# Kernel optimization log

Measured on AMD Instinct MI355X. Metric: run time of the kernel, lower is better.

The kernel has to match this reference:

```python
import jax, jax.numpy as jnp
import numpy as np

N = 100000   # num nodes
E = 2000000  # num edges
D = 32       # feature dim (input_dim == hidden)
L = 6        # num layers
R = 50       # num relations
B = 64       # num query source nodes
EPS = 1e-6


def setup_inputs() -> dict:
    key = jax.random.key(0)
    ks = jax.random.split(key, 7)
    edge_index = jax.random.randint(ks[0], (E, 2), 0, N)
    edge_type = jax.random.randint(ks[1], (E,), 0, R)
    edge_weight = jnp.ones((E,), jnp.float32)
    h_index = jax.random.randint(ks[2], (B,), 0, N)
    rel_emb = jax.random.normal(ks[3], (L, R, D), jnp.float32) * 0.1
    W = jax.random.normal(ks[4], (L, 13 * D, D), jnp.float32) * (1.0 / np.sqrt(13 * D))
    b = jnp.zeros((L, D), jnp.float32)
    return dict(edge_index=edge_index, edge_type=edge_type, edge_weight=edge_weight,
                h_index=h_index, rel_emb=rel_emb, W=W, b=b)


def _layer(x, boundary, node_in, node_out, edge_type, edge_weight, rel, W, b, degree_out):
    # message: distmult  (E, D)
    msg = x[node_in] * rel[edge_type]
    # append boundary as self-loop messages -> (E+N, D)
    msg = jnp.concatenate([msg, boundary], axis=0)
    seg = jnp.concatenate([node_out, jnp.arange(N)], axis=0)
    w = jnp.concatenate([edge_weight, jnp.ones((N,), x.dtype)], axis=0)[:, None]
    mw = msg * w
    cnt = jax.ops.segment_sum(jnp.ones_like(w), seg, num_segments=N)  # (N,1), >=1
    mean = jax.ops.segment_sum(mw, seg, num_segments=N) / cnt
    sq_mean = jax.ops.segment_sum((msg * msg) * w, seg, num_segments=N) / cnt
    mx = jax.ops.segment_max(mw, seg, num_segments=N)
    mn = jax.ops.segment_min(mw, seg, num_segments=N)
    std = jnp.sqrt(jnp.clip(sq_mean - mean * mean, EPS, None))
    # interleave per-channel [mean, max, min, std] -> (N, 4D)
    feat = jnp.stack([mean, mx, mn, std], axis=-1).reshape(N, 4 * D)
    scale = jnp.log(degree_out)              # (N, 1)
    scale = scale / scale.mean()
    scales = jnp.concatenate([jnp.ones_like(scale), scale,
                              1.0 / jnp.clip(scale, 1e-2, None)], axis=-1)  # (N, 3)
    update = (feat[:, :, None] * scales[:, None, :]).reshape(N, 12 * D)
    out = jnp.concatenate([x, update], axis=-1) @ W + b  # (N, D)
    return jax.nn.relu(out)


def reference(edge_index, edge_type, edge_weight, h_index, rel_emb, W, b):
    node_in = edge_index[:, 0]
    node_out = edge_index[:, 1]
    boundary = jnp.zeros((N, D), jnp.float32).at[h_index].set(1.0)
    degree_out = (jax.ops.segment_sum(edge_weight, node_out, num_segments=N) + 1.0)[:, None]
    x = boundary
    for i in range(L):
        x = _layer(x, boundary, node_in, node_out, edge_type, edge_weight,
                   rel_emb[i], W[i], b[i], degree_out)
    return x  # node_feature (N, D)
```

## Files before the change

### kernel.cpp

```cpp
#include <hip/hip_runtime.h>
#include <math.h>

#define NN 100000
#define EE 2000000
#define DD 32
#define LL 6
#define RR 50
#define BB 64
#define SCAN_BLK 98


typedef __attribute__((ext_vector_type(8))) short bf16x8;
typedef __attribute__((ext_vector_type(4))) float f32x4;

__device__ __forceinline__ unsigned short f2bf(float f) {
    unsigned int u = __float_as_uint(f);
    u = (u + 0x7FFFu + ((u >> 16) & 1u)) >> 16;
    return (unsigned short)u;
}
__device__ __forceinline__ float bf2f(unsigned short h) {
    return __uint_as_float((unsigned int)h << 16);
}

__global__ void hist_kernel(const int* __restrict__ ei, int* __restrict__ cnt) {
    for (int e = blockIdx.x * blockDim.x + threadIdx.x; e < EE; e += gridDim.x * blockDim.x)
        atomicAdd(&cnt[ei[2 * e + 1]], 1);
}

__global__ void boundary_kernel(const int* __restrict__ h, float* __restrict__ bnd,
                                float* __restrict__ x0, unsigned short* __restrict__ xbf0) {
    int t = blockIdx.x * blockDim.x + threadIdx.x;
    if (t >= BB * DD) return;
    int bidx = t >> 5, d = t & 31;
    int node = h[bidx];
    x0[node * DD + d] = 1.0f;
    if (xbf0) xbf0[node * DD + d] = 0x3F80;
    if (d == 0) bnd[node] = 1.0f;
}

__global__ void scanA_kernel(const int* __restrict__ cnt, int* __restrict__ rowptr,
                             int* __restrict__ bsum) {
    __shared__ int sh[1024];
    const int idx = blockIdx.x * 1024 + threadIdx.x;
    const int v = (idx < NN) ? cnt[idx] : 0;
    sh[threadIdx.x] = v;
    __syncthreads();
    for (int off = 1; off < 1024; off <<= 1) {
        int t = (threadIdx.x >= (unsigned)off) ? sh[threadIdx.x - off] : 0;
        __syncthreads();
        sh[threadIdx.x] += t;
        __syncthreads();
    }
    if (idx < NN) rowptr[idx] = sh[threadIdx.x] - v;
    if (threadIdx.x == 1023) bsum[blockIdx.x] = sh[1023];
}

__global__ void scanB_kernel(const int* __restrict__ bsum, int* __restrict__ boff,
                             int* __restrict__ rowptr) {
    __shared__ int sh[128];
    const int t = threadIdx.x;
    const int v = (t < SCAN_BLK) ? bsum[t] : 0;
    sh[t] = v;
    __syncthreads();
    for (int off = 1; off < 128; off <<= 1) {
        int u = (t >= off) ? sh[t - off] : 0;
        __syncthreads();
        sh[t] += u;
        __syncthreads();
    }
    if (t < SCAN_BLK) boff[t] = sh[t] - v;
    if (t == SCAN_BLK - 1) rowptr[NN] = sh[t];
}

__global__ void scanC_kernel(int* __restrict__ rowptr, int* __restrict__ cursor,
                             const int* __restrict__ boff) {
    const int idx = blockIdx.x * 1024 + threadIdx.x;
    if (idx < NN) {
        const int r = rowptr[idx] + boff[blockIdx.x];
        rowptr[idx] = r;
        cursor[idx] = r;
    }
}

__global__ void logsum_kernel(const int* __restrict__ cnt, double* __restrict__ out) {
    __shared__ double sh[256];
    double local = 0.0;
    for (int i = blockIdx.x * blockDim.x + threadIdx.x; i < NN; i += gridDim.x * blockDim.x)
        local += log((double)cnt[i] + 1.0);
    sh[threadIdx.x] = local;
    __syncthreads();
    for (int o = 128; o > 0; o >>= 1) {
        if (threadIdx.x < (unsigned)o) sh[threadIdx.x] += sh[threadIdx.x + o];
        __syncthreads();
    }
    if (threadIdx.x == 0) atomicAdd(out, sh[0]);
}

__global__ void scalefin_kernel(const int* __restrict__ cnt, const double* __restrict__ logsum,
                                float* __restrict__ scalev, float* __restrict__ iscalev) {
    float mean = (float)(logsum[0] / (double)NN);
    for (int i = blockIdx.x * blockDim.x + threadIdx.x; i < NN; i += gridDim.x * blockDim.x) {
        float s = logf((float)cnt[i] + 1.0f) / mean;
        scalev[i] = s;
        iscalev[i] = 1.0f / fmaxf(s, 0.01f);
    }
}

__global__ void scatter_kernel(const int* __restrict__ ei, const int* __restrict__ et,
                               int* __restrict__ cursor, int* __restrict__ recs) {
    for (int e = blockIdx.x * blockDim.x + threadIdx.x; e < EE; e += gridDim.x * blockDim.x) {
        int nin = ei[2 * e];
        int nout = ei[2 * e + 1];
        int pos = atomicAdd(&cursor[nout], 1);
        recs[pos] = (nin << 6) | et[e];
    }
}

__global__ __launch_bounds__(256, 4) void aggbf_kernel(
    const unsigned short* __restrict__ xbf, float* __restrict__ feat,
    const int* __restrict__ recs, const int* __restrict__ rowptr,
    const float* __restrict__ bnd, const float* __restrict__ rel_l) {
    __shared__ float rel_s[RR * 32];
    {
        const float4* r4 = (const float4*)rel_l;
        float4* rs4 = (float4*)rel_s;
        for (int i = threadIdx.x; i < (RR * 32) / 4; i += 256) rs4[i] = r4[i];
    }
    __syncthreads();

    const int lane = threadIdx.x & 63;
    const int half = lane >> 5;
    const int d = lane & 31;
    const int wid = blockIdx.x * 4 + (threadIdx.x >> 6);
    const int nwaves = gridDim.x * 4;

    for (int n0 = wid * 2; n0 < NN; n0 += nwaves * 2) {
        const int nA = n0, nB = n0 + 1;
        const int rowA = rowptr[nA], endA = rowptr[nA + 1];
        const int rowB = rowptr[nB], endB = rowptr[nB + 1];
        const float bvA = bnd[nA], bvB = bnd[nB];

        float sA = (half == 0) ? bvA : 0.f, qA = sA;
        float mxA = bvA, mnA = bvA;
        float sB = (half == 0) ? bvB : 0.f, qB = sB;
        float mxB = bvB, mnB = bvB;

        int eA = rowA + half, eB = rowB + half;

#define ACC_A(M) { sA += (M); qA = fmaf((M), (M), qA); mxA = fmaxf(mxA, (M)); mnA = fminf(mnA, (M)); }
#define ACC_B(M) { sB += (M); qB = fmaf((M), (M), qB); mxB = fmaxf(mxB, (M)); mnB = fminf(mnB, (M)); }
#define MSG(P) (bf2f(xbf[((P) >> 6) * DD + d]) * rel_s[((P) & 63) * DD + d])

        while (eA + 6 < endA && eB + 6 < endB) {
            const int pa0 = recs[eA], pa1 = recs[eA + 2], pa2 = recs[eA + 4], pa3 = recs[eA + 6];
            const int pb0 = recs[eB], pb1 = recs[eB + 2], pb2 = recs[eB + 4], pb3 = recs[eB + 6];
            const float ma0 = MSG(pa0), ma1 = MSG(pa1), ma2 = MSG(pa2), ma3 = MSG(pa3);
            const float mb0 = MSG(pb0), mb1 = MSG(pb1), mb2 = MSG(pb2), mb3 = MSG(pb3);
            ACC_A(ma0); ACC_A(ma1); ACC_A(ma2); ACC_A(ma3);
            ACC_B(mb0); ACC_B(mb1); ACC_B(mb2); ACC_B(mb3);
            eA += 8; eB += 8;
        }
        while (eA + 2 < endA) {
            const int pa0 = recs[eA], pa1 = recs[eA + 2];
            const float ma0 = MSG(pa0), ma1 = MSG(pa1);
            ACC_A(ma0); ACC_A(ma1);
            eA += 4;
        }
        while (eB + 2 < endB) {
            const int pb0 = recs[eB], pb1 = recs[eB + 2];
            const float mb0 = MSG(pb0), mb1 = MSG(pb1);
            ACC_B(mb0); ACC_B(mb1);
            eB += 4;
        }
        if (eA < endA) { const float m0 = MSG(recs[eA]); ACC_A(m0); }
        if (eB < endB) { const float m0 = MSG(recs[eB]); ACC_B(m0); }
#undef MSG
#undef ACC_A
#undef ACC_B

        sA += __shfl_xor(sA, 32); qA += __shfl_xor(qA, 32);
        mxA = fmaxf(mxA, __shfl_xor(mxA, 32)); mnA = fminf(mnA, __shfl_xor(mnA, 32));
        sB += __shfl_xor(sB, 32); qB += __shfl_xor(qB, 32);
        mxB = fmaxf(mxB, __shfl_xor(mxB, 32)); mnB = fminf(mnB, __shfl_xor(mnB, 32));

        const float invA = 1.0f / (float)(endA - rowA + 1);
        const float invB = 1.0f / (float)(endB - rowB + 1);
        if (half == 0) {
            const float mean = sA * invA;
            const float stdv = sqrtf(fmaxf(qA * invA - mean * mean, 1e-6f));
            float* fb = feat + (size_t)nA * 128;
            fb[d] = mean; fb[32 + d] = mxA; fb[64 + d] = mnA; fb[96 + d] = stdv;
        } else {
            const float mean = sB * invB;
            const float stdv = sqrtf(fmaxf(qB * invB - mean * mean, 1e-6f));
            float* fb = feat + (size_t)nB * 128;
            fb[d] = mean; fb[32 + d] = mxB; fb[64 + d] = mnB; fb[96 + d] = stdv;
        }
    }
}

__global__ __launch_bounds__(256, 4) void agg_kernel(
    const float* __restrict__ xin, float* __restrict__ feat,
    const int* __restrict__ recs, const int* __restrict__ rowptr,
    const float* __restrict__ bnd, const float* __restrict__ rel_l) {
    __shared__ float rel_s[RR * 32];
    {
        const float4* r4 = (const float4*)rel_l;
        float4* rs4 = (float4*)rel_s;
        for (int i = threadIdx.x; i < (RR * 32) / 4; i += 256) rs4[i] = r4[i];
    }
    __syncthreads();

    const int lane = threadIdx.x & 63;
    const int half = lane >> 5;
    const int d = lane & 31;
    const int wid = blockIdx.x * 4 + (threadIdx.x >> 6);
    const int nwaves = gridDim.x * 4;

    for (int n0 = wid * 2; n0 < NN; n0 += nwaves * 2) {
        const int nA = n0, nB = n0 + 1;
        const int rowA = rowptr[nA], endA = rowptr[nA + 1];
        const int rowB = rowptr[nB], endB = rowptr[nB + 1];
        const float bvA = bnd[nA], bvB = bnd[nB];

        float sA = (half == 0) ? bvA : 0.f, qA = sA;
        float mxA = bvA, mnA = bvA;
        float sB = (half == 0) ? bvB : 0.f, qB = sB;
        float mxB = bvB, mnB = bvB;

        int eA = rowA + half, eB = rowB + half;
#define STEP_A { const int p0_ = recs[eA]; const int p1_ = recs[eA + 2];                  \
        const float m0_ = xin[(p0_ >> 6) * DD + d] * rel_s[(p0_ & 63) * DD + d];           \
        const float m1_ = xin[(p1_ >> 6) * DD + d] * rel_s[(p1_ & 63) * DD + d];           \
        sA += m0_; qA = fmaf(m0_, m0_, qA); mxA = fmaxf(mxA, m0_); mnA = fminf(mnA, m0_);  \
        sA += m1_; qA = fmaf(m1_, m1_, qA); mxA = fmaxf(mxA, m1_); mnA = fminf(mnA, m1_);  \
        eA += 4; }
#define STEP_B { const int p0_ = recs[eB]; const int p1_ = recs[eB + 2];                  \
        const float m0_ = xin[(p0_ >> 6) * DD + d] * rel_s[(p0_ & 63) * DD + d];           \
        const float m1_ = xin[(p1_ >> 6) * DD + d] * rel_s[(p1_ & 63) * DD + d];           \
        sB += m0_; qB = fmaf(m0_, m0_, qB); mxB = fmaxf(mxB, m0_); mnB = fminf(mnB, m0_);  \
        sB += m1_; qB = fmaf(m1_, m1_, qB); mxB = fmaxf(mxB, m1_); mnB = fminf(mnB, m1_);  \
        eB += 4; }
        while (eA + 2 < endA && eB + 2 < endB) { STEP_A; STEP_B; }
        while (eA + 2 < endA) { STEP_A; }
        while (eB + 2 < endB) { STEP_B; }
#undef STEP_A
#undef STEP_B
        if (eA < endA) {
            const int p0_ = recs[eA];
            const float m0_ = xin[(p0_ >> 6) * DD + d] * rel_s[(p0_ & 63) * DD + d];
            sA += m0_; qA = fmaf(m0_, m0_, qA); mxA = fmaxf(mxA, m0_); mnA = fminf(mnA, m0_);
        }
        if (eB < endB) {
            const int p0_ = recs[eB];
            const float m0_ = xin[(p0_ >> 6) * DD + d] * rel_s[(p0_ & 63) * DD + d];
            sB += m0_; qB = fmaf(m0_, m0_, qB); mxB = fmaxf(mxB, m0_); mnB = fminf(mnB, m0_);
        }

        sA += __shfl_xor(sA, 32); qA += __shfl_xor(qA, 32);
        mxA = fmaxf(mxA, __shfl_xor(mxA, 32)); mnA = fminf(mnA, __shfl_xor(mnA, 32));
        sB += __shfl_xor(sB, 32); qB += __shfl_xor(qB, 32);
        mxB = fmaxf(mxB, __shfl_xor(mxB, 32)); mnB = fminf(mnB, __shfl_xor(mnB, 32));

        const float invA = 1.0f / (float)(endA - rowA + 1);
        const float invB = 1.0f / (float)(endB - rowB + 1);
        if (half == 0) {
            const float mean = sA * invA;
            const float stdv = sqrtf(fmaxf(qA * invA - mean * mean, 1e-6f));
            float* fb = feat + (size_t)nA * 128;
            fb[d] = mean; fb[32 + d] = mxA; fb[64 + d] = mnA; fb[96 + d] = stdv;
        } else {
            const float mean = sB * invB;
            const float stdv = sqrtf(fmaxf(qB * invB - mean * mean, 1e-6f));
            float* fb = feat + (size_t)nB * 128;
            fb[d] = mean; fb[32 + d] = mxB; fb[64 + d] = mnB; fb[96 + d] = stdv;
        }
    }
}

__global__ __launch_bounds__(256, 2) void epmm_kernel(
    const float* __restrict__ xin, const float* __restrict__ feat,
    float* __restrict__ xout, unsigned short* __restrict__ xbf_out,
    const float* __restrict__ scalev, const float* __restrict__ iscalev,
    const float* __restrict__ Wl, const float* __restrict__ bl) {
    __shared__ unsigned short Wf[13 * 2 * 64 * 8];
    __shared__ unsigned short off_sel[416];
    __shared__ float b_s[32];
    __shared__ unsigned short stage[4][16 * 161];

    for (int idx = threadIdx.x; idx < 13 * 2 * 64 * 8; idx += 256) {
        const int i = idx & 7, l = (idx >> 3) & 63, h = (idx >> 9) & 1, kk = idx >> 10;
        const int k = kk * 32 + (l >> 4) * 8 + i;
        const int col = h * 16 + (l & 15);
        Wf[idx] = f2bf(Wl[k * 32 + col]);
    }
    for (int k = threadIdx.x; k < 416; k += 256) {
        unsigned short os;
        if (k < 32) os = (unsigned short)k;
        else {
            const int d = (k - 32) / 12, r = (k - 32) % 12, kf = r / 3, s = r % 3;
            os = (unsigned short)((32 + kf * 32 + d) | (s << 8));
        }
        off_sel[k] = os;
    }
    if (threadIdx.x < 32) b_s[threadIdx.x] = bl[threadIdx.x];
    __syncthreads();

    const int lane = threadIdx.x & 63;
    const int wslot = threadIdx.x >> 6;
    const int wid = blockIdx.x * 4 + wslot;
    const int nwaves = gridDim.x * 4;
    unsigned short* stg = &stage[wslot][0];
    const int arow = lane & 15;
    const int kg = lane >> 4;
    const int ccol = lane & 15;

    for (int tile = wid; tile < NN / 16; tile += nwaves) {
        const int base = tile * 16;
        for (int idx = lane; idx < 512; idx += 64) {
            const int rr = idx >> 5, c = idx & 31;
            stg[rr * 161 + c] = f2bf(xin[(base + rr) * DD + c]);
        }
        for (int idx = lane; idx < 2048; idx += 64) {
            const int rr = idx >> 7, c = idx & 127;
            stg[rr * 161 + 32 + c] = f2bf(feat[(size_t)(base + rr) * 128 + c]);
        }
        const float sclR = scalev[base + arow], isclR = iscalev[base + arow];
        const unsigned short* srow = &stg[arow * 161];

        f32x4 acc0 = {0.f, 0.f, 0.f, 0.f}, acc1 = {0.f, 0.f, 0.f, 0.f};
#pragma unroll
        for (int kk = 0; kk < 13; kk++) {
            bf16x8 a;
#pragma unroll
            for (int i = 0; i < 8; i++) {
                const int k = kk * 32 + kg * 8 + i;
                const unsigned short os = off_sel[k];
                const int off = os & 255;
                const int s = os >> 8;
                float v = bf2f(srow[off]);
                v = (s == 0) ? v : (s == 1 ? v * sclR : v * isclR);
                a[i] = (short)f2bf(v);
            }
            const bf16x8 b0 = *(const bf16x8*)&Wf[((kk * 2 + 0) * 64 + lane) * 8];
            const bf16x8 b1 = *(const bf16x8*)&Wf[((kk * 2 + 1) * 64 + lane) * 8];
            acc0 = __builtin_amdgcn_mfma_f32_16x16x32_bf16(a, b0, acc0, 0, 0, 0);
            acc1 = __builtin_amdgcn_mfma_f32_16x16x32_bf16(a, b1, acc1, 0, 0, 0);
        }
#pragma unroll
        for (int r = 0; r < 4; r++) {
            const int orow = base + kg * 4 + r;
            const float v0 = fmaxf(acc0[r] + b_s[ccol], 0.0f);
            const float v1 = fmaxf(acc1[r] + b_s[ccol + 16], 0.0f);
            xout[orow * DD + ccol] = v0;
            xout[orow * DD + ccol + 16] = v1;
            if (xbf_out) {
                xbf_out[orow * DD + ccol] = f2bf(v0);
                xbf_out[orow * DD + ccol + 16] = f2bf(v1);
            }
        }
    }
}

__global__ __launch_bounds__(512, 2) void fused_kernel(
    const float* __restrict__ xin, float* __restrict__ xout,
    const int* __restrict__ recs, const int* __restrict__ rowptr,
    const float* __restrict__ bnd, const float* __restrict__ scalev,
    const float* __restrict__ iscalev,
    const float* __restrict__ Wl, const float* __restrict__ bl,
    const float* __restrict__ rel_l) {
    __shared__ float W_s[416 * 32];
    __shared__ float rel_s[RR * 32];
    __shared__ float b_s[32];
    {
        const float4* w4 = (const float4*)Wl;
        float4* ws4 = (float4*)W_s;
        for (int i = threadIdx.x; i < (416 * 32) / 4; i += 512) ws4[i] = w4[i];
        const float4* r4 = (const float4*)rel_l;
        float4* rs4 = (float4*)rel_s;
        for (int i = threadIdx.x; i < (RR * 32) / 4; i += 512) rs4[i] = r4[i];
        if (threadIdx.x < 32) b_s[threadIdx.x] = bl[threadIdx.x];
    }
    __syncthreads();

    const int lane = threadIdx.x & 63;
    const int half = lane >> 5;
    const int d = lane & 31;
    const int wid = blockIdx.x * 8 + (threadIdx.x >> 6);
    const int nwaves = gridDim.x * 8;

    for (int n0 = wid * 2; n0 < NN; n0 += nwaves * 2) {
        const int nA = n0, nB = n0 + 1;
        const int rowA = rowptr[nA], endA = rowptr[nA + 1];
        const int rowB = rowptr[nB], endB = rowptr[nB + 1];
        const float bvA = bnd[nA], bvB = bnd[nB];
        const float sclA = scalev[nA], isclA = iscalev[nA];
        const float sclB = scalev[nB], isclB = iscalev[nB];
        const float xvA = xin[nA * DD + d], xvB = xin[nB * DD + d];

        float sA = (half == 0) ? bvA : 0.f, qA = sA;
        float mxA = bvA, mnA = bvA;
        float sB = (half == 0) ? bvB : 0.f, qB = sB;
        float mxB = bvB, mnB = bvB;

        int eA = rowA + half, eB = rowB + half;
#define STEP_A { const int p0_ = recs[eA]; const int p1_ = recs[eA + 2];                  \
        const float m0_ = xin[(p0_ >> 6) * DD + d] * rel_s[(p0_ & 63) * DD + d];           \
        const float m1_ = xin[(p1_ >> 6) * DD + d] * rel_s[(p1_ & 63) * DD + d];           \
        sA += m0_; qA = fmaf(m0_, m0_, qA); mxA = fmaxf(mxA, m0_); mnA = fminf(mnA, m0_);  \
        sA += m1_; qA = fmaf(m1_, m1_, qA); mxA = fmaxf(mxA, m1_); mnA = fminf(mnA, m1_);  \
        eA += 4; }
#define STEP_B { const int p0_ = recs[eB]; const int p1_ = recs[eB + 2];                  \
        const float m0_ = xin[(p0_ >> 6) * DD + d] * rel_s[(p0_ & 63) * DD + d];           \
        const float m1_ = xin[(p1_ >> 6) * DD + d] * rel_s[(p1_ & 63) * DD + d];           \
        sB += m0_; qB = fmaf(m0_, m0_, qB); mxB = fmaxf(mxB, m0_); mnB = fminf(mnB, m0_);  \
        sB += m1_; qB = fmaf(m1_, m1_, qB); mxB = fmaxf(mxB, m1_); mnB = fminf(mnB, m1_);  \
        eB += 4; }
        while (eA + 2 < endA && eB + 2 < endB) { STEP_A; STEP_B; }
        while (eA + 2 < endA) { STEP_A; }
        while (eB + 2 < endB) { STEP_B; }
#undef STEP_A
#undef STEP_B
        if (eA < endA) {
            const int p0_ = recs[eA];
            const float m0_ = xin[(p0_ >> 6) * DD + d] * rel_s[(p0_ & 63) * DD + d];
            sA += m0_; qA = fmaf(m0_, m0_, qA); mxA = fmaxf(mxA, m0_); mnA = fminf(mnA, m0_);
        }
        if (eB < endB) {
            const int p0_ = recs[eB];
            const float m0_ = xin[(p0_ >> 6) * DD + d] * rel_s[(p0_ & 63) * DD + d];
            sB += m0_; qB = fmaf(m0_, m0_, qB); mxB = fmaxf(mxB, m0_); mnB = fminf(mnB, m0_);
        }

        sA += __shfl_xor(sA, 32); qA += __shfl_xor(qA, 32);
        mxA = fmaxf(mxA, __shfl_xor(mxA, 32)); mnA = fminf(mnA, __shfl_xor(mnA, 32));
        sB += __shfl_xor(sB, 32); qB += __shfl_xor(qB, 32);
        mxB = fmaxf(mxB, __shfl_xor(mxB, 32)); mnB = fminf(mnB, __shfl_xor(mnB, 32));

        const float invA = 1.0f / (float)(endA - rowA + 1);
        const float invB = 1.0f / (float)(endB - rowB + 1);
        const float meanA = sA * invA;
        const float stdA = sqrtf(fmaxf(qA * invA - meanA * meanA, 1e-6f));
        const float meanB = sB * invB;
        const float stdB = sqrtf(fmaxf(qB * invB - meanB * meanB, 1e-6f));

        float xv[2] = {xvA, xvB};
        float f0[2] = {meanA, meanB}, f1[2] = {mxA, mxB};
        float f2[2] = {mnA, mnB}, f3[2] = {stdA, stdB};
        float aX[2] = {0.f, 0.f}, aA[2] = {0.f, 0.f}, aB[2] = {0.f, 0.f}, aC[2] = {0.f, 0.f};
        const int srcBase = half * 48;
#pragma unroll
        for (int t = 0; t < 16; t++) {
            const int src = srcBase + t;
            const int i = half * 16 + t;
            const float w0 = W_s[i * 32 + d];
            const float* wr = &W_s[(32 + i * 12) * 32 + d];
            const float w1 = wr[0 * 32], w2 = wr[1 * 32], w3 = wr[2 * 32];
            const float w4 = wr[3 * 32], w5 = wr[4 * 32], w6 = wr[5 * 32];
            const float w7 = wr[6 * 32], w8 = wr[7 * 32], w9 = wr[8 * 32];
            const float wa = wr[9 * 32], wb = wr[10 * 32], wc = wr[11 * 32];
#pragma unroll
            for (int p = 0; p < 2; p++) {
                const float xb = __shfl(xv[p], src);
                const float g0 = __shfl(f0[p], src);
                const float g1 = __shfl(f1[p], src);
                const float g2 = __shfl(f2[p], src);
                const float g3 = __shfl(f3[p], src);
                aX[p] = fmaf(xb, w0, aX[p]);
                aA[p] = fmaf(g0, w1, aA[p]); aB[p] = fmaf(g0, w2, aB[p]); aC[p] = fmaf(g0, w3, aC[p]);
                aA[p] = fmaf(g1, w4, aA[p]); aB[p] = fmaf(g1, w5, aB[p]); aC[p] = fmaf(g1, w6, aC[p]);
                aA[p] = fmaf(g2, w7, aA[p]); aB[p] = fmaf(g2, w8, aB[p]); aC[p] = fmaf(g2, w9, aC[p]);
                aA[p] = fmaf(g3, wa, aA[p]); aB[p] = fmaf(g3, wb, aB[p]); aC[p] = fmaf(g3, wc, aC[p]);
            }
        }
        float rA = aX[0] + aA[0] + sclA * aB[0] + isclA * aC[0];
        float rB = aX[1] + aA[1] + sclB * aB[1] + isclB * aC[1];
        rA += __shfl_xor(rA, 32);
        rB += __shfl_xor(rB, 32);
        rA = fmaxf(rA + b_s[d], 0.0f);
        rB = fmaxf(rB + b_s[d], 0.0f);
        if (half == 0) {
            xout[nA * DD + d] = rA;
            xout[nB * DD + d] = rB;
        }
    }
}

extern "C" void kernel_launch(void* const* d_in, const int* in_sizes, int n_in,
                              void* d_out, int out_size, void* d_ws, size_t ws_size,
                              hipStream_t stream) {
    const int* ei = (const int*)d_in[0];
    const int* et = (const int*)d_in[1];
    const int* hidx = (const int*)d_in[3];
    const float* rel = (const float*)d_in[4];
    const float* W = (const float*)d_in[5];
    const float* b = (const float*)d_in[6];

    char* ws = (char*)d_ws;
    int* cnt = (int*)(ws + 0);
    int* rowptr = (int*)(ws + 400000);
    int* cursor = (int*)(ws + 800016);
    float* scalev = (float*)(ws + 1200016);
    float* iscalev = (float*)(ws + 1600016);
    float* bnd = (float*)(ws + 2000016);
    double* logsum = (double*)(ws + 2400016);
    int* bsum = (int*)(ws + 2400032);
    int* boff = (int*)(ws + 2400544);
    int* recs = (int*)(ws + 2401056);

    const bool bf = (ws_size >= (size_t)100001088);
    const bool split = bf || (ws_size >= (size_t)87201088);
    float* feat = (float*)(ws + 10401088);
    float* xbuf0 = split ? (float*)(ws + 61601088) : (float*)(ws + 10401088);
    float* xbuf1 = split ? (float*)(ws + 74401088) : (float*)(ws + 23201088);
    unsigned short* xbf0 = bf ? (unsigned short*)(ws + 87201088) : nullptr;
    unsigned short* xbf1 = bf ? (unsigned short*)(ws + 93601088) : nullptr;

    hipMemsetAsync(ws, 0, 2400032, stream);
    hipMemsetAsync(recs + EE, 0, 8 * sizeof(int), stream);
    hipMemsetAsync(xbuf0, 0, NN * DD * sizeof(float), stream);
    if (bf) hipMemsetAsync(xbf0, 0, NN * DD * sizeof(unsigned short), stream);

    hist_kernel<<<1024, 256, 0, stream>>>(ei, cnt);
    boundary_kernel<<<(BB * DD + 255) / 256, 256, 0, stream>>>(hidx, bnd, xbuf0, xbf0);
    scanA_kernel<<<SCAN_BLK, 1024, 0, stream>>>(cnt, rowptr, bsum);
    scanB_kernel<<<1, 128, 0, stream>>>(bsum, boff, rowptr);
    scanC_kernel<<<SCAN_BLK, 1024, 0, stream>>>(rowptr, cursor, boff);
    logsum_kernel<<<256, 256, 0, stream>>>(cnt, logsum);
    scalefin_kernel<<<400, 256, 0, stream>>>(cnt, logsum, scalev, iscalev);
    scatter_kernel<<<1024, 256, 0, stream>>>(ei, et, cursor, recs);

    float* xout_final = (float*)d_out;
    for (int l = 0; l < LL; l++) {
        const float* xin = (l % 2 == 0) ? xbuf0 : xbuf1;
        float* xout = (l == LL - 1) ? xout_final : ((l % 2 == 0) ? xbuf1 : xbuf0);
        const float* Wl = W + (size_t)l * 416 * 32;
        const float* bl = b + (size_t)l * 32;
        const float* rl = rel + (size_t)l * RR * 32;
        if (bf) {
            unsigned short* xbf_in = (l % 2 == 0) ? xbf0 : xbf1;
            unsigned short* xbf_out = (l == LL - 1) ? nullptr : ((l % 2 == 0) ? xbf1 : xbf0);
            aggbf_kernel<<<2048, 256, 0, stream>>>(xbf_in, feat, recs, rowptr, bnd, rl);
            epmm_kernel<<<1024, 256, 0, stream>>>(xin, feat, xout, xbf_out, scalev, iscalev, Wl, bl);
        } else if (split) {
            agg_kernel<<<2048, 256, 0, stream>>>(xin, feat, recs, rowptr, bnd, rl);
            epmm_kernel<<<1024, 256, 0, stream>>>(xin, feat, xout, nullptr, scalev, iscalev, Wl, bl);
        } else {
            fused_kernel<<<512, 512, 0, stream>>>(
                xin, xout, recs, rowptr, bnd, scalev, iscalev, Wl, bl, rl);
        }
    }
}
```

Baseline: 864.8 us.

## Replace global edge scatter with two-pass bucketed binning by destination block

The single scatter pass, which did random atomics and writes over all N destination cursors, becomes two passes. The first bins edges into 64-node buckets using per-bucket atomic cursors. The second places the records of each bucket with one block per bucket, so cursor atomics and record writes stay within a small, cache-local range. This should improve locality of the CSR build, at the cost of an extra pass over 2M records and a temporary buffer that aliases the feat region.

```diff
diff --git a/kernel.cpp b/kernel.cpp
--- a/kernel.cpp
+++ b/kernel.cpp
@@ -8,6 +8,7 @@
 #define RR 50
 #define BB 64
 #define SCAN_BLK 98
+#define BUCKETS 1563
 
 
 typedef __attribute__((ext_vector_type(8))) short bf16x8;
@@ -103,6 +104,36 @@
         float s = logf((float)cnt[i] + 1.0f) / mean;
         scalev[i] = s;
         iscalev[i] = 1.0f / fmaxf(s, 0.01f);
+    }
+}
+
+__global__ void binbase_kernel(const int* __restrict__ rowptr, int* __restrict__ bcur) {
+    const int b = blockIdx.x * blockDim.x + threadIdx.x;
+    if (b < BUCKETS) bcur[b] = rowptr[b * 64];
+}
+
+__global__ void bin_kernel(const int* __restrict__ ei, const int* __restrict__ et,
+                           int* __restrict__ bcur, int* __restrict__ binrecs) {
+    for (int e = blockIdx.x * blockDim.x + threadIdx.x; e < EE; e += gridDim.x * blockDim.x) {
+        const int src = ei[2 * e];
+        const int dst = ei[2 * e + 1];
+        const int b = dst >> 6;
+        const int pos = atomicAdd(&bcur[b], 1);
+        binrecs[pos] = ((dst & 63) << 23) | (src << 6) | et[e];
+    }
+}
+
+__global__ void scatter2_kernel(const int* __restrict__ binrecs, const int* __restrict__ rowptr,
+                                int* __restrict__ cursor, int* __restrict__ recs) {
+    const int b = blockIdx.x;
+    const int lo = rowptr[b * 64];
+    const int hiIdx = (b + 1) * 64;
+    const int hi = rowptr[(hiIdx < NN) ? hiIdx : NN];
+    for (int i = lo + threadIdx.x; i < hi; i += blockDim.x) {
+        const int r = binrecs[i];
+        const int dst = (b << 6) + (r >> 23);
+        const int pos = atomicAdd(&cursor[dst], 1);
+        recs[pos] = r & 0x7FFFFF;
     }
 }
 
@@ -511,6 +542,8 @@
     const bool bf = (ws_size >= (size_t)100001088);
     const bool split = bf || (ws_size >= (size_t)87201088);
     float* feat = (float*)(ws + 10401088);
+    int* binrecs = (int*)(ws + 10401088);
+    int* bcur = (int*)(ws + 10401088 + 8000000);
     float* xbuf0 = split ? (float*)(ws + 61601088) : (float*)(ws + 10401088);
     float* xbuf1 = split ? (float*)(ws + 74401088) : (float*)(ws + 23201088);
     unsigned short* xbf0 = bf ? (unsigned short*)(ws + 87201088) : nullptr;
@@ -528,7 +561,13 @@
     scanC_kernel<<<SCAN_BLK, 1024, 0, stream>>>(rowptr, cursor, boff);
     logsum_kernel<<<256, 256, 0, stream>>>(cnt, logsum);
     scalefin_kernel<<<400, 256, 0, stream>>>(cnt, logsum, scalev, iscalev);
-    scatter_kernel<<<1024, 256, 0, stream>>>(ei, et, cursor, recs);
+    if (split) {
+        binbase_kernel<<<(BUCKETS + 255) / 256, 256, 0, stream>>>(rowptr, bcur);
+        bin_kernel<<<1024, 256, 0, stream>>>(ei, et, bcur, binrecs);
+        scatter2_kernel<<<BUCKETS, 256, 0, stream>>>(binrecs, rowptr, cursor, recs);
+    } else {
+        scatter_kernel<<<1024, 256, 0, stream>>>(ei, et, cursor, recs);
+    }
 
     float* xout_final = (float*)d_out;
     for (int l = 0; l < LL; l++) {
```

Result: slower. 1.068 ms (+23.5%).
